# Kernel optimization log

Hardware: AMD Instinct MI355X
Metric: run time of the kernel (lower is better)

## Reference

```python
import jax, jax.numpy as jnp
import numpy as np

N = 50000      # nodes
E = 800000     # edges (before self-loops)
DIN = 256      # in_channel
H = 1          # heads (PyG GATConv default)
C = 128        # out_channel per head
NEG_SLOPE = 0.2


def setup_inputs() -> dict:
    key = jax.random.key(0)
    k1, k2, k3, k4, k5 = jax.random.split(key, 5)
    x = jax.random.normal(k1, (N, DIN), jnp.float32)
    # random edges guaranteed to have no self-loops (PyG removes then re-adds them)
    src = jax.random.randint(k2, (E,), 0, N, dtype=jnp.int32)
    off = jax.random.randint(k3, (E,), 1, N, dtype=jnp.int32)
    dst = (src + off) % N
    edge_index = jnp.stack([src, dst])  # [2, E], row0=source j, row1=target i
    W = jax.random.normal(k4, (DIN, H * C), jnp.float32) / np.sqrt(DIN)
    att = jax.random.normal(k5, (1, H, 2 * C), jnp.float32) * 0.1
    bias = jnp.zeros((H * C,), jnp.float32)
    return {"x": x, "edge_index": edge_index, "W": W, "att": att, "bias": bias}


def reference(x, edge_index, W, att, bias):
    n = x.shape[0]
    h = (x @ W).reshape(n, H, C)                       # [N,H,C]
    # add self-loops (PyG GATConv forward)
    loops = jnp.arange(n, dtype=edge_index.dtype)
    src = jnp.concatenate([edge_index[0], loops])       # [Et]
    dst = jnp.concatenate([edge_index[1], loops])       # [Et]
    h_i = h[dst]                                        # [Et,H,C] target feats
    h_j = h[src]                                        # [Et,H,C] source feats
    # per-edge attention logit: sum(cat(x_i, x_j) * att)
    alpha = jnp.sum(jnp.concatenate([h_i, h_j], axis=-1) * att, axis=-1)  # [Et,H]
    alpha = jax.nn.leaky_relu(alpha, NEG_SLOPE)
    # segment softmax grouped by destination node (numerically stable)
    amax = jax.ops.segment_max(alpha, dst, num_segments=n)  # [N,H]
    ex = jnp.exp(alpha - amax[dst])
    denom = jax.ops.segment_sum(ex, dst, num_segments=n)    # [N,H]
    a = ex / (denom[dst] + 1e-16)                            # [Et,H]
    # scatter-aggregate weighted source features to targets
    out = jax.ops.segment_sum(h_j * a[..., None], dst, num_segments=n)  # [N,H,C]
    return out.reshape(n, H * C) + bias
```

## Files before the change

### kernel.cpp

```cpp
#include <hip/hip_runtime.h>
#include <hip/hip_bf16.h>

constexpr int N_NODES = 50000;
constexpr int DIN     = 256;
constexpr int C_OUT   = 128;
constexpr int E_EDGES = 800000;
constexpr int ET      = E_EDGES + N_NODES;
constexpr float NEG_SLOPE = 0.2f;

constexpr int GEMM_RPB    = 128;
constexpr int GEMM_BLOCKS = (N_NODES + GEMM_RPB - 1) / GEMM_RPB;
constexpr int LINK_EPB    = 2048;
constexpr int LINK_BLOCKS = (ET + LINK_EPB - 1) / LINK_EPB;

typedef __attribute__((ext_vector_type(8))) short short8v;
typedef __attribute__((ext_vector_type(4))) float f32x4;

static __device__ __forceinline__ ushort f2bf(float f) {
    __hip_bfloat16 b = __float2bfloat16(f);
    return *reinterpret_cast<ushort*>(&b);
}
static __device__ __forceinline__ short f2bfs(float f) {
    __hip_bfloat16 b = __float2bfloat16(f);
    return *reinterpret_cast<short*>(&b);
}

__global__ void wconv_kernel(const float* __restrict__ W, ushort* __restrict__ wt,
                             int* __restrict__ head) {
    const int idx = blockIdx.x * 256 + threadIdx.x;
    if (idx < DIN * C_OUT) {
        const int k = idx >> 7, col = idx & 127;
        const int ks = k >> 5, kgrp = (k >> 3) & 3, j = k & 7;
        const int c = col >> 4, col16 = col & 15;
        const int fragpos = ((ks * 8 + c) * 64 + kgrp * 16 + col16) * 8 + j;
        wt[fragpos] = f2bf(W[idx]);
    }
    if (idx < N_NODES) head[idx] = -1;
}

__global__ __launch_bounds__(256) void gemm_link(const float* __restrict__ x,
                                                 const ushort* __restrict__ wt,
                                                 const float* __restrict__ att,
                                                 const int* __restrict__ ei,
                                                 ushort* __restrict__ hb,
                                                 float* __restrict__ s_dst,
                                                 float* __restrict__ s_src,
                                                 int* __restrict__ head,
                                                 int* __restrict__ nxt) {
    __shared__ ushort lw[DIN * C_OUT];
    const int t = threadIdx.x;

    if (blockIdx.x >= GEMM_BLOCKS) {
        const int b = blockIdx.x - GEMM_BLOCKS;
        #pragma unroll
        for (int i = 0; i < 8; i++) {
            const int e = b * LINK_EPB + i * 256 + t;
            if (e < ET) {
                const int d = (e < E_EDGES) ? ei[E_EDGES + e] : (e - E_EDGES);
                nxt[e] = atomicExch(&head[d], e);
            }
        }
        return;
    }

    {
        const uint4* src = (const uint4*)wt;
        uint4* dst = (uint4*)lw;
        #pragma unroll
        for (int i = 0; i < 16; i++) dst[t + i * 256] = src[t + i * 256];
    }
    __syncthreads();

    const int lane = t & 63, wv = t >> 6;
    const int col16 = lane & 15, kgrp = lane >> 4;
    const int rowbase = blockIdx.x * GEMM_RPB + wv * 32;
    int r0 = rowbase + col16;      if (r0 >= N_NODES) r0 = N_NODES - 1;
    int r1 = rowbase + 16 + col16; if (r1 >= N_NODES) r1 = N_NODES - 1;
    const float* xr0 = x + (size_t)r0 * DIN + kgrp * 8;
    const float* xr1 = x + (size_t)r1 * DIN + kgrp * 8;

    f32x4 acc[2][8] = {};
    const short8v* lwf = (const short8v*)lw;
    #pragma unroll
    for (int ks = 0; ks < 8; ks++) {
        const float4 v0 = *(const float4*)(xr0 + ks * 32);
        const float4 v1 = *(const float4*)(xr0 + ks * 32 + 4);
        const float4 u0 = *(const float4*)(xr1 + ks * 32);
        const float4 u1 = *(const float4*)(xr1 + ks * 32 + 4);
        short8v a0, a1;
        a0[0] = f2bfs(v0.x); a0[1] = f2bfs(v0.y); a0[2] = f2bfs(v0.z); a0[3] = f2bfs(v0.w);
        a0[4] = f2bfs(v1.x); a0[5] = f2bfs(v1.y); a0[6] = f2bfs(v1.z); a0[7] = f2bfs(v1.w);
        a1[0] = f2bfs(u0.x); a1[1] = f2bfs(u0.y); a1[2] = f2bfs(u0.z); a1[3] = f2bfs(u0.w);
        a1[4] = f2bfs(u1.x); a1[5] = f2bfs(u1.y); a1[6] = f2bfs(u1.z); a1[7] = f2bfs(u1.w);
        #pragma unroll
        for (int c = 0; c < 8; c++) {
            const short8v bfr = lwf[(ks * 8 + c) * 64 + lane];
            acc[0][c] = __builtin_amdgcn_mfma_f32_16x16x32_bf16(a0, bfr, acc[0][c], 0, 0, 0);
            acc[1][c] = __builtin_amdgcn_mfma_f32_16x16x32_bf16(a1, bfr, acc[1][c], 0, 0, 0);
        }
    }

    float attd[8], atts[8];
    #pragma unroll
    for (int c = 0; c < 8; c++) {
        attd[c] = att[c * 16 + col16];
        atts[c] = att[C_OUT + c * 16 + col16];
    }
    #pragma unroll
    for (int rs = 0; rs < 2; rs++) {
        #pragma unroll
        for (int j = 0; j < 4; j++) {
            const int row = rowbase + rs * 16 + kgrp * 4 + j;
            const bool ok = (row < N_NODES);
            float pd = 0.f, ps = 0.f;
            #pragma unroll
            for (int c = 0; c < 8; c++) {
                const float hv = acc[rs][c][j];
                pd += hv * attd[c];
                ps += hv * atts[c];
                if (ok) hb[(size_t)row * C_OUT + c * 16 + col16] = f2bf(hv);
            }
            #pragma unroll
            for (int off = 1; off < 16; off <<= 1) {
                pd += __shfl_xor(pd, off);
                ps += __shfl_xor(ps, off);
            }
            if (col16 == 0 && ok) { s_dst[row] = pd; s_src[row] = ps; }
        }
    }
}

__global__ __launch_bounds__(256) void aggregate_kernel(
    const ushort* __restrict__ hb, const int* __restrict__ head,
    const int* __restrict__ nxt, const int* __restrict__ ei,
    const float* __restrict__ s_dst, const float* __restrict__ s_src,
    const float* __restrict__ bias, float* __restrict__ out) {
    const int t = threadIdx.x;
    const int wv = t >> 6, lane = t & 63;
    const int sub = lane >> 4, l16 = lane & 15;
    const int node = blockIdx.x * 16 + wv * 4 + sub;

    const float sd = s_dst[node];
    int e = head[node];
    float den = 0.f;
    float acc[8] = {};
    const uint4* __restrict__ h4 = (const uint4*)hb;

    while (__ballot(e >= 0)) {
        if (e >= 0) {
            const int nx = nxt[e];
            const int s = (e < E_EDGES) ? ei[e] : (e - E_EDGES);
            float a = sd + s_src[s];
            a = (a > 0.f) ? a : NEG_SLOPE * a;
            const float w = __expf(a);
            den += w;
            const uint4 hv = h4[(size_t)s * 16 + l16];
            acc[0] += w * __uint_as_float(hv.x << 16);
            acc[1] += w * __uint_as_float(hv.x & 0xffff0000u);
            acc[2] += w * __uint_as_float(hv.y << 16);
            acc[3] += w * __uint_as_float(hv.y & 0xffff0000u);
            acc[4] += w * __uint_as_float(hv.z << 16);
            acc[5] += w * __uint_as_float(hv.z & 0xffff0000u);
            acc[6] += w * __uint_as_float(hv.w << 16);
            acc[7] += w * __uint_as_float(hv.w & 0xffff0000u);
            e = nx;
        }
    }
    const float inv = 1.f / (den + 1e-16f);
    const float4 b0 = *(const float4*)(bias + l16 * 8);
    const float4 b1 = *(const float4*)(bias + l16 * 8 + 4);
    float4 o0 = make_float4(acc[0] * inv + b0.x, acc[1] * inv + b0.y,
                            acc[2] * inv + b0.z, acc[3] * inv + b0.w);
    float4 o1 = make_float4(acc[4] * inv + b1.x, acc[5] * inv + b1.y,
                            acc[6] * inv + b1.z, acc[7] * inv + b1.w);
    *(float4*)(out + (size_t)node * C_OUT + l16 * 8)     = o0;
    *(float4*)(out + (size_t)node * C_OUT + l16 * 8 + 4) = o1;
}

extern "C" void kernel_launch(void* const* d_in, const int* in_sizes, int n_in,
                              void* d_out, int out_size, void* d_ws, size_t ws_size,
                              hipStream_t stream) {
    const float* x    = (const float*)d_in[0];
    const int*   ei   = (const int*)d_in[1];
    const float* W    = (const float*)d_in[2];
    const float* att  = (const float*)d_in[3];
    const float* bias = (const float*)d_in[4];
    float* out = (float*)d_out;

    ushort* wt    = (ushort*)d_ws;
    ushort* hbuf  = wt + DIN * C_OUT;
    float*  s_src = (float*)(hbuf + (size_t)N_NODES * C_OUT);
    float*  s_dst = s_src + N_NODES;
    int*    head  = (int*)(s_dst + N_NODES);
    int*    nxt   = head + N_NODES;

    wconv_kernel<<<(N_NODES + 255) / 256, 256, 0, stream>>>(W, wt, head);
    gemm_link<<<GEMM_BLOCKS + LINK_BLOCKS, 256, 0, stream>>>(
        x, wt, att, ei, hbuf, s_dst, s_src, head, nxt);
    aggregate_kernel<<<N_NODES / 16, 256, 0, stream>>>(
        hbuf, head, nxt, ei, s_dst, s_src, bias, out);
}
```

Measured before the change: 107.5 us.

## Split link/GEMM kernels, pack next+src, halve LDS, widen aggregation per node

The fused gemm+link launch becomes two kernels. The link kernel stores (next, src) pairs as int2, so aggregation gets the source index in the same load as the next pointer instead of a separate gather from edge_index. The GEMM stages W in LDS in two halves, cutting shared memory from 64KB to 32KB to allow more resident blocks, at the cost of an extra barrier and reload. Aggregation now has 8 lanes per node, each handling 16 channels with two loads, so each wave walks 8 lists at once; this adds a launch and loses the overlap of the link and GEMM work.

```diff
diff --git a/kernel.cpp b/kernel.cpp
--- a/kernel.cpp
+++ b/kernel.cpp
@@ -12,6 +12,8 @@
 constexpr int GEMM_BLOCKS = (N_NODES + GEMM_RPB - 1) / GEMM_RPB;
 constexpr int LINK_EPB    = 2048;
 constexpr int LINK_BLOCKS = (ET + LINK_EPB - 1) / LINK_EPB;
+constexpr int AGG_NPB     = 32;
+constexpr int AGG_BLOCKS  = (N_NODES + AGG_NPB - 1) / AGG_NPB;
 
 typedef __attribute__((ext_vector_type(8))) short short8v;
 typedef __attribute__((ext_vector_type(4))) float f32x4;
@@ -38,39 +40,31 @@
     if (idx < N_NODES) head[idx] = -1;
 }
 
-__global__ __launch_bounds__(256) void gemm_link(const float* __restrict__ x,
+__global__ __launch_bounds__(256) void link_kernel(const int* __restrict__ ei,
+                                                   int* __restrict__ head,
+                                                   int2* __restrict__ nxt2) {
+    const int b = blockIdx.x;
+    #pragma unroll
+    for (int i = 0; i < 8; i++) {
+        const int e = b * LINK_EPB + i * 256 + threadIdx.x;
+        if (e < ET) {
+            int s, d;
+            if (e < E_EDGES) { s = ei[e]; d = ei[E_EDGES + e]; }
+            else             { s = e - E_EDGES; d = s; }
+            const int old = atomicExch(&head[d], e);
+            nxt2[e] = make_int2(old, s);
+        }
+    }
+}
+
+__global__ __launch_bounds__(256) void gemm_mfma(const float* __restrict__ x,
                                                  const ushort* __restrict__ wt,
                                                  const float* __restrict__ att,
-                                                 const int* __restrict__ ei,
                                                  ushort* __restrict__ hb,
                                                  float* __restrict__ s_dst,
-                                                 float* __restrict__ s_src,
-                                                 int* __restrict__ head,
-                                                 int* __restrict__ nxt) {
-    __shared__ ushort lw[DIN * C_OUT];
+                                                 float* __restrict__ s_src) {
+    __shared__ ushort lw[DIN * C_OUT / 2];
     const int t = threadIdx.x;
-
-    if (blockIdx.x >= GEMM_BLOCKS) {
-        const int b = blockIdx.x - GEMM_BLOCKS;
-        #pragma unroll
-        for (int i = 0; i < 8; i++) {
-            const int e = b * LINK_EPB + i * 256 + t;
-            if (e < ET) {
-                const int d = (e < E_EDGES) ? ei[E_EDGES + e] : (e - E_EDGES);
-                nxt[e] = atomicExch(&head[d], e);
-            }
-        }
-        return;
-    }
-
-    {
-        const uint4* src = (const uint4*)wt;
-        uint4* dst = (uint4*)lw;
-        #pragma unroll
-        for (int i = 0; i < 16; i++) dst[t + i * 256] = src[t + i * 256];
-    }
-    __syncthreads();
-
     const int lane = t & 63, wv = t >> 6;
     const int col16 = lane & 15, kgrp = lane >> 4;
     const int rowbase = blockIdx.x * GEMM_RPB + wv * 32;
@@ -82,21 +76,33 @@
     f32x4 acc[2][8] = {};
     const short8v* lwf = (const short8v*)lw;
     #pragma unroll
-    for (int ks = 0; ks < 8; ks++) {
-        const float4 v0 = *(const float4*)(xr0 + ks * 32);
-        const float4 v1 = *(const float4*)(xr0 + ks * 32 + 4);
-        const float4 u0 = *(const float4*)(xr1 + ks * 32);
-        const float4 u1 = *(const float4*)(xr1 + ks * 32 + 4);
-        short8v a0, a1;
-        a0[0] = f2bfs(v0.x); a0[1] = f2bfs(v0.y); a0[2] = f2bfs(v0.z); a0[3] = f2bfs(v0.w);
-        a0[4] = f2bfs(v1.x); a0[5] = f2bfs(v1.y); a0[6] = f2bfs(v1.z); a0[7] = f2bfs(v1.w);
-        a1[0] = f2bfs(u0.x); a1[1] = f2bfs(u0.y); a1[2] = f2bfs(u0.z); a1[3] = f2bfs(u0.w);
-        a1[4] = f2bfs(u1.x); a1[5] = f2bfs(u1.y); a1[6] = f2bfs(u1.z); a1[7] = f2bfs(u1.w);
+    for (int ph = 0; ph < 2; ph++) {
+        if (ph) __syncthreads();
+        {
+            const uint4* src = (const uint4*)(wt + ph * (DIN * C_OUT / 2));
+            uint4* dst = (uint4*)lw;
+            #pragma unroll
+            for (int i = 0; i < 8; i++) dst[t + i * 256] = src[t + i * 256];
+        }
+        __syncthreads();
         #pragma unroll
-        for (int c = 0; c < 8; c++) {
-            const short8v bfr = lwf[(ks * 8 + c) * 64 + lane];
-            acc[0][c] = __builtin_amdgcn_mfma_f32_16x16x32_bf16(a0, bfr, acc[0][c], 0, 0, 0);
-            acc[1][c] = __builtin_amdgcn_mfma_f32_16x16x32_bf16(a1, bfr, acc[1][c], 0, 0, 0);
+        for (int ks = 0; ks < 4; ks++) {
+            const int kg = ph * 4 + ks;
+            const float4 v0 = *(const float4*)(xr0 + kg * 32);
+            const float4 v1 = *(const float4*)(xr0 + kg * 32 + 4);
+            const float4 u0 = *(const float4*)(xr1 + kg * 32);
+            const float4 u1 = *(const float4*)(xr1 + kg * 32 + 4);
+            short8v a0, a1;
+            a0[0] = f2bfs(v0.x); a0[1] = f2bfs(v0.y); a0[2] = f2bfs(v0.z); a0[3] = f2bfs(v0.w);
+            a0[4] = f2bfs(v1.x); a0[5] = f2bfs(v1.y); a0[6] = f2bfs(v1.z); a0[7] = f2bfs(v1.w);
+            a1[0] = f2bfs(u0.x); a1[1] = f2bfs(u0.y); a1[2] = f2bfs(u0.z); a1[3] = f2bfs(u0.w);
+            a1[4] = f2bfs(u1.x); a1[5] = f2bfs(u1.y); a1[6] = f2bfs(u1.z); a1[7] = f2bfs(u1.w);
+            #pragma unroll
+            for (int c = 0; c < 8; c++) {
+                const short8v bfr = lwf[(ks * 8 + c) * 64 + lane];
+                acc[0][c] = __builtin_amdgcn_mfma_f32_16x16x32_bf16(a0, bfr, acc[0][c], 0, 0, 0);
+                acc[1][c] = __builtin_amdgcn_mfma_f32_16x16x32_bf16(a1, bfr, acc[1][c], 0, 0, 0);
+            }
         }
     }
 
@@ -132,49 +138,65 @@
 
 __global__ __launch_bounds__(256) void aggregate_kernel(
     const ushort* __restrict__ hb, const int* __restrict__ head,
-    const int* __restrict__ nxt, const int* __restrict__ ei,
-    const float* __restrict__ s_dst, const float* __restrict__ s_src,
-    const float* __restrict__ bias, float* __restrict__ out) {
+    const int2* __restrict__ nxt2, const float* __restrict__ s_dst,
+    const float* __restrict__ s_src, const float* __restrict__ bias,
+    float* __restrict__ out) {
     const int t = threadIdx.x;
     const int wv = t >> 6, lane = t & 63;
-    const int sub = lane >> 4, l16 = lane & 15;
-    const int node = blockIdx.x * 16 + wv * 4 + sub;
-
-    const float sd = s_dst[node];
-    int e = head[node];
+    const int sub = lane >> 3, l8 = lane & 7;
+    const int node = blockIdx.x * AGG_NPB + wv * 8 + sub;
+    const bool valid = (node < N_NODES);
+
+    const float sd = valid ? s_dst[node] : 0.f;
+    int e = valid ? head[node] : -1;
     float den = 0.f;
-    float acc[8] = {};
+    float acc[16] = {};
     const uint4* __restrict__ h4 = (const uint4*)hb;
 
     while (__ballot(e >= 0)) {
         if (e >= 0) {
-            const int nx = nxt[e];
-            const int s = (e < E_EDGES) ? ei[e] : (e - E_EDGES);
+            const int2 ns = nxt2[e];
+            const int s = ns.y;
+            e = ns.x;
             float a = sd + s_src[s];
             a = (a > 0.f) ? a : NEG_SLOPE * a;
             const float w = __expf(a);
             den += w;
-            const uint4 hv = h4[(size_t)s * 16 + l16];
-            acc[0] += w * __uint_as_float(hv.x << 16);
-            acc[1] += w * __uint_as_float(hv.x & 0xffff0000u);
-            acc[2] += w * __uint_as_float(hv.y << 16);
-            acc[3] += w * __uint_as_float(hv.y & 0xffff0000u);
-            acc[4] += w * __uint_as_float(hv.z << 16);
-            acc[5] += w * __uint_as_float(hv.z & 0xffff0000u);
-            acc[6] += w * __uint_as_float(hv.w << 16);
-            acc[7] += w * __uint_as_float(hv.w & 0xffff0000u);
-            e = nx;
-        }
-    }
+            const uint4 hv0 = h4[(size_t)s * 16 + l8];
+            const uint4 hv1 = h4[(size_t)s * 16 + 8 + l8];
+            acc[0]  += w * __uint_as_float(hv0.x << 16);
+            acc[1]  += w * __uint_as_float(hv0.x & 0xffff0000u);
+            acc[2]  += w * __uint_as_float(hv0.y << 16);
+            acc[3]  += w * __uint_as_float(hv0.y & 0xffff0000u);
+            acc[4]  += w * __uint_as_float(hv0.z << 16);
+            acc[5]  += w * __uint_as_float(hv0.z & 0xffff0000u);
+            acc[6]  += w * __uint_as_float(hv0.w << 16);
+            acc[7]  += w * __uint_as_float(hv0.w & 0xffff0000u);
+            acc[8]  += w * __uint_as_float(hv1.x << 16);
+            acc[9]  += w * __uint_as_float(hv1.x & 0xffff0000u);
+            acc[10] += w * __uint_as_float(hv1.y << 16);
+            acc[11] += w * __uint_as_float(hv1.y & 0xffff0000u);
+            acc[12] += w * __uint_as_float(hv1.z << 16);
+            acc[13] += w * __uint_as_float(hv1.z & 0xffff0000u);
+            acc[14] += w * __uint_as_float(hv1.w << 16);
+            acc[15] += w * __uint_as_float(hv1.w & 0xffff0000u);
+        }
+    }
+    if (!valid) return;
     const float inv = 1.f / (den + 1e-16f);
-    const float4 b0 = *(const float4*)(bias + l16 * 8);
-    const float4 b1 = *(const float4*)(bias + l16 * 8 + 4);
-    float4 o0 = make_float4(acc[0] * inv + b0.x, acc[1] * inv + b0.y,
-                            acc[2] * inv + b0.z, acc[3] * inv + b0.w);
-    float4 o1 = make_float4(acc[4] * inv + b1.x, acc[5] * inv + b1.y,
-                            acc[6] * inv + b1.z, acc[7] * inv + b1.w);
-    *(float4*)(out + (size_t)node * C_OUT + l16 * 8)     = o0;
-    *(float4*)(out + (size_t)node * C_OUT + l16 * 8 + 4) = o1;
+    float* op = out + (size_t)node * C_OUT;
+    #pragma unroll
+    for (int half = 0; half < 2; half++) {
+        const int base = half * 64 + l8 * 8;
+        const float4 b0 = *(const float4*)(bias + base);
+        const float4 b1 = *(const float4*)(bias + base + 4);
+        float4 o0 = make_float4(acc[half * 8 + 0] * inv + b0.x, acc[half * 8 + 1] * inv + b0.y,
+                                acc[half * 8 + 2] * inv + b0.z, acc[half * 8 + 3] * inv + b0.w);
+        float4 o1 = make_float4(acc[half * 8 + 4] * inv + b1.x, acc[half * 8 + 5] * inv + b1.y,
+                                acc[half * 8 + 6] * inv + b1.z, acc[half * 8 + 7] * inv + b1.w);
+        *(float4*)(op + base)     = o0;
+        *(float4*)(op + base + 4) = o1;
+    }
 }
 
 extern "C" void kernel_launch(void* const* d_in, const int* in_sizes, int n_in,
@@ -192,11 +214,11 @@
     float*  s_src = (float*)(hbuf + (size_t)N_NODES * C_OUT);
     float*  s_dst = s_src + N_NODES;
     int*    head  = (int*)(s_dst + N_NODES);
-    int*    nxt   = head + N_NODES;
+    int2*   nxt2  = (int2*)(head + N_NODES);
 
     wconv_kernel<<<(N_NODES + 255) / 256, 256, 0, stream>>>(W, wt, head);
-    gemm_link<<<GEMM_BLOCKS + LINK_BLOCKS, 256, 0, stream>>>(
-        x, wt, att, ei, hbuf, s_dst, s_src, head, nxt);
-    aggregate_kernel<<<N_NODES / 16, 256, 0, stream>>>(
-        hbuf, head, nxt, ei, s_dst, s_src, bias, out);
-}
+    link_kernel<<<LINK_BLOCKS, 256, 0, stream>>>(ei, head, nxt2);
+    gemm_mfma<<<GEMM_BLOCKS, 256, 0, stream>>>(x, wt, att, hbuf, s_dst, s_src);
+    aggregate_kernel<<<AGG_BLOCKS, 256, 0, stream>>>(
+        hbuf, head, nxt2, s_dst, s_src, bias, out);
+}
```

New measurement: 112.5 us. 1.05x slower.
